# Kernel tuning notes

Measured on AMD Instinct MI355X. Metric: run time of the kernel, lower is better.

Reference implementation:

```python
import jax, jax.numpy as jnp
import numpy as np
import math

B, L, D, H = 16, 512, 128, 8


def setup_inputs() -> dict:
    key = jax.random.key(0)
    ks = jax.random.split(key, 10)
    xavier = lambda k, shp: jax.random.normal(k, shp, jnp.float32) * math.sqrt(2.0 / (shp[0] + shp[1]))
    inp = {
        "x": jax.random.normal(ks[0], (B, L, D), jnp.float32),
        "W_q": xavier(ks[1], (H * D, D)),
        "b_q": jnp.zeros((H * D,), jnp.float32),
        "W_k": xavier(ks[2], (H * D, D)),
        "b_k": jnp.zeros((H * D,), jnp.float32),
        "W_v": xavier(ks[3], (H * D, D)),
        "b_v": jnp.zeros((H * D,), jnp.float32),
        "W_o": xavier(ks[4], (D, H * D)),
        "b_o": jnp.zeros((D,), jnp.float32),
        "pad_mask": jax.random.randint(ks[5], (B, L, L), 0, 2).astype(bool),
        "batch_size": B,
        "max_len": L,
    }
    return inp


def reference(x, W_q, b_q, W_k, b_k, W_v, b_v, W_o, b_o, pad_mask, batch_size, max_len):
    # project: [B, L, D] -> [B, L, H*D] -> head-major [H*B, L, D]
    def proj(W, b):
        y = jnp.einsum('bld,ed->ble', x, W) + b          # [B, L, H*D]
        y = y.reshape(batch_size, max_len, H, D)
        return y.transpose(2, 0, 1, 3).reshape(H * batch_size, max_len, D)

    q = proj(W_q, b_q)
    k = proj(W_k, b_k)
    v = proj(W_v, b_v)

    scores = jnp.einsum('nqd,nkd->nqk', q, k)            # [H*B, L, L]
    mask = jnp.tile(pad_mask, (H, 1, 1))                 # repeat(n_heads,1,1)
    # faithful quirk: mask BEFORE scaling, softmax over QUERY axis (dim=1)
    scores = jnp.where(mask, -1e9, scores) / math.sqrt(D)
    attn = jax.nn.softmax(scores, axis=1)
    att = jnp.einsum('nqk,nkd->nqd', attn, v)            # [H*B, L, D]
    # faithful quirk: torch .view from (H*B, L, D) to (B, L, H*D)
    att = att.reshape(batch_size, max_len, H * D)
    out = jnp.einsum('ble,de->bld', att, W_o) + b_o      # [B, L, D]
    return out
```

## Files before the change

kernel.cpp:

```cpp
#include <hip/hip_runtime.h>

#define B_  16
#define L_  512
#define D_  128
#define H_  8
#define HD_ 1024
#define NH_ 128
#define M_  8192

typedef unsigned short u16;
typedef __attribute__((ext_vector_type(8))) short s16x8;
typedef __attribute__((ext_vector_type(4))) float f32x4;

__device__ __forceinline__ float bf2f(u16 u) {
    union { unsigned u; float f; } x; x.u = ((unsigned)u) << 16; return x.f;
}
__device__ __forceinline__ u16 f2bf(float f) {
    unsigned u = __float_as_uint(f);
    return (u16)((u + 0x7FFFu + ((u >> 16) & 1u)) >> 16);
}

__device__ __forceinline__ void mfma_bt64(const u16* __restrict__ A, int lda,
                                          const u16* __restrict__ B, int ldb,
                                          int K, int lane, f32x4 acc[4][4]) {
    const int mr = lane & 15, quad = lane >> 4;
    for (int k0 = 0; k0 < K; k0 += 32) {
        s16x8 av[4], bv[4];
#pragma unroll
        for (int i = 0; i < 4; i++)
            av[i] = *(const s16x8*)(A + (size_t)(i * 16 + mr) * lda + k0 + quad * 8);
#pragma unroll
        for (int j = 0; j < 4; j++)
            bv[j] = *(const s16x8*)(B + (size_t)(j * 16 + mr) * ldb + k0 + quad * 8);
#pragma unroll
        for (int i = 0; i < 4; i++)
#pragma unroll
            for (int j = 0; j < 4; j++)
                acc[i][j] = __builtin_amdgcn_mfma_f32_16x16x32_bf16(av[i], bv[j], acc[i][j], 0, 0, 0);
    }
}

__global__ void k0_detect(const unsigned int* __restrict__ pad,
                          const unsigned int* __restrict__ xw,
                          int* __restrict__ flags) {
    __shared__ int sMask, sCnt;
    if (threadIdx.x == 0) { sMask = 0; sCnt = 0; }
    __syncthreads();
    int bad = 0;
#pragma unroll
    for (int i = 0; i < 4; i++) {
        unsigned u = pad[threadIdx.x * 4 + i];
        bad |= (u > 1u) ? 1 : 0;
    }
    int cnt = 0;
#pragma unroll
    for (int i = 0; i < 16; i++) {
        unsigned w = xw[threadIdx.x * 16 + i];
        unsigned e = (w >> 7) & 0xFFu;
        cnt += (e >= 100u && e <= 131u) ? 1 : 0;
    }
    if (bad) atomicOr(&sMask, 1);
    atomicAdd(&sCnt, cnt);
    __syncthreads();
    if (threadIdx.x == 0) {
        flags[0] = (sCnt > 2048) ? 1 : 0;
        flags[1] = sMask;
    }
}

#define PREP_TOT 1576064
__global__ __launch_bounds__(256) void kprep_conv(
    const void* x, const void* Wq, const void* bq, const void* Wk, const void* bk,
    const void* Wv, const void* bv, const void* Wo, const void* bo,
    const int* __restrict__ flags,
    u16* xb, u16* Wqb, u16* Wkb, u16* Wvb, u16* Wob,
    u16* bqb, u16* bkb, u16* bvb, u16* bob) {
    int gid = blockIdx.x * 256 + threadIdx.x;
    if (gid >= PREP_TOT) return;
    const int dt = flags[0];
    const void* src; u16* dst; int off;
    if      (gid < 1048576) { src = x;  dst = xb;  off = gid; }
    else if (gid < 1179648) { src = Wq; dst = Wqb; off = gid - 1048576; }
    else if (gid < 1310720) { src = Wk; dst = Wkb; off = gid - 1179648; }
    else if (gid < 1441792) { src = Wv; dst = Wvb; off = gid - 1310720; }
    else if (gid < 1572864) { src = Wo; dst = Wob; off = gid - 1441792; }
    else if (gid < 1573888) { src = bq; dst = bqb; off = gid - 1572864; }
    else if (gid < 1574912) { src = bk; dst = bkb; off = gid - 1573888; }
    else if (gid < 1575936) { src = bv; dst = bvb; off = gid - 1574912; }
    else                    { src = bo; dst = bob; off = gid - 1575936; }
    dst[off] = dt ? ((const u16*)src)[off] : f2bf(((const float*)src)[off]);
}

__global__ __launch_bounds__(256) void kprep_mask(const void* __restrict__ pad,
                                                  const int* __restrict__ flags,
                                                  unsigned* __restrict__ mb) {
    int w = blockIdx.x * 256 + threadIdx.x;
    size_t base = (size_t)w * 32;
    unsigned m = 0;
    if (flags[1]) {
        const unsigned char* p = (const unsigned char*)pad;
#pragma unroll
        for (int b = 0; b < 32; b++) m |= (p[base + b] ? 1u : 0u) << b;
    } else {
        const int* p = (const int*)pad;
#pragma unroll
        for (int b = 0; b < 32; b++) m |= (p[base + b] ? 1u : 0u) << b;
    }
    mb[w] = m;
}

__global__ __launch_bounds__(256) void k1_proj(
    const u16* __restrict__ xb,
    const u16* __restrict__ Wqb, const u16* __restrict__ Wkb, const u16* __restrict__ Wvb,
    const u16* __restrict__ bqb, const u16* __restrict__ bkb, const u16* __restrict__ bvb,
    u16* __restrict__ qb, u16* __restrict__ kb, u16* __restrict__ vtb) {
    const int h  = blockIdx.x;
    const int m0 = blockIdx.y * 128;
    const int z  = blockIdx.z;
    const u16* W    = (z == 0) ? Wqb : (z == 1) ? Wkb : Wvb;
    const u16* bias = (z == 0) ? bqb : (z == 1) ? bkb : bvb;

    const int lane = threadIdx.x & 63, wave = threadIdx.x >> 6;
    const int wr = wave >> 1, wc = wave & 1;
    const int mr = lane & 15, quad = lane >> 4;

    f32x4 acc[4][4];
#pragma unroll
    for (int i = 0; i < 4; i++)
#pragma unroll
        for (int j = 0; j < 4; j++) acc[i][j] = (f32x4){0.f, 0.f, 0.f, 0.f};

    mfma_bt64(xb + (size_t)(m0 + wr * 64) * D_, D_,
              W + (size_t)(h * 128 + wc * 64) * D_, D_, D_, lane, acc);

    __shared__ __align__(16) u16 T[128][144];
#pragma unroll
    for (int i = 0; i < 4; i++)
#pragma unroll
        for (int j = 0; j < 4; j++) {
            int col = wc * 64 + j * 16 + mr;
            float bv_ = bf2f(bias[h * 128 + col]);
#pragma unroll
            for (int r = 0; r < 4; r++)
                T[wr * 64 + i * 16 + quad * 4 + r][col] = f2bf(acc[i][j][r] + bv_);
        }
    __syncthreads();

    const int bb = m0 >> 9, l0 = m0 & 511;
    const int t = threadIdx.x;
    if (z < 2) {
        u16* out = z ? kb : qb;
        int row = t >> 1, c0 = (t & 1) * 64;
        u16* dst = out + ((size_t)(h * B_ + bb) * L_ + l0 + row) * D_ + c0;
#pragma unroll
        for (int c = 0; c < 64; c += 8)
            *(uint4*)(dst + c) = *(const uint4*)&T[row][c0 + c];
    } else {
        int d = t >> 1, lc0 = (t & 1) * 64;
        u16* dst = vtb + ((size_t)(h * B_ + bb) * D_ + d) * L_ + l0 + lc0;
#pragma unroll
        for (int c = 0; c < 64; c += 8) {
            u16 tmp[8];
#pragma unroll
            for (int s = 0; s < 8; s++) tmp[s] = T[lc0 + c + s][d];
            *(uint4*)(dst + c) = *(const uint4*)tmp;
        }
    }
}

__global__ __launch_bounds__(256) void k2_scores(
    const u16* __restrict__ qb, const u16* __restrict__ kb,
    const unsigned* __restrict__ mbits,
    u16* __restrict__ sb, float* __restrict__ linv) {
    const int k0g = blockIdx.x * 128;
    const int n   = blockIdx.y;
    const int bb  = n & (B_ - 1);
    const int lane = threadIdx.x & 63, wave = threadIdx.x >> 6;
    const int wr = wave >> 1, wc = wave & 1;
    const int mr = lane & 15, quad = lane >> 4;
    const float rs = 0.08838834764831845f;

    __shared__ __align__(16) u16 T[128][144];
    __shared__ float CS[2][128];

    const u16* Abase = qb + (size_t)n * L_ * D_;
    const u16* Bbase = kb + (size_t)n * L_ * D_ + (size_t)(k0g + wc * 64) * D_;

    float colsum[4] = {0.f, 0.f, 0.f, 0.f};
    for (int qt = 0; qt < 4; qt++) {
        f32x4 acc[4][4];
#pragma unroll
        for (int i = 0; i < 4; i++)
#pragma unroll
            for (int j = 0; j < 4; j++) acc[i][j] = (f32x4){0.f, 0.f, 0.f, 0.f};

        mfma_bt64(Abase + (size_t)(qt * 128 + wr * 64) * D_, D_, Bbase, D_, D_, lane, acc);

#pragma unroll
        for (int i = 0; i < 4; i++)
#pragma unroll
            for (int j = 0; j < 4; j++) {
                int kc = k0g + wc * 64 + j * 16 + mr;
#pragma unroll
                for (int r = 0; r < 4; r++) {
                    int ql = wr * 64 + i * 16 + quad * 4 + r;
                    int q  = qt * 128 + ql;
                    unsigned w = mbits[((size_t)(bb << 9) + q) * 16 + (kc >> 5)];
                    float s = ((w >> (kc & 31)) & 1u) ? -1e9f : acc[i][j][r];
                    float e = __expf(s * rs);
                    colsum[j] += e;
                    T[ql][wc * 64 + j * 16 + mr] = f2bf(e);
                }
            }
        __syncthreads();
        {
            int t = threadIdx.x, row = t >> 1, c0 = (t & 1) * 64;
            u16* dst = sb + ((size_t)n * L_ + qt * 128 + row) * L_ + k0g + c0;
#pragma unroll
            for (int c = 0; c < 64; c += 8)
                *(uint4*)(dst + c) = *(const uint4*)&T[row][c0 + c];
        }
        __syncthreads();
    }
#pragma unroll
    for (int j = 0; j < 4; j++) {
        colsum[j] += __shfl_xor(colsum[j], 16);
        colsum[j] += __shfl_xor(colsum[j], 32);
    }
    if (quad == 0) {
#pragma unroll
        for (int j = 0; j < 4; j++) CS[wr][wc * 64 + j * 16 + mr] = colsum[j];
    }
    __syncthreads();
    if (threadIdx.x < 128)
        linv[(size_t)n * L_ + k0g + threadIdx.x] =
            1.0f / (CS[0][threadIdx.x] + CS[1][threadIdx.x]);
}

__global__ __launch_bounds__(256) void k3_vscale(u16* __restrict__ vtb,
                                                 const float* __restrict__ linv) {
    int idx = blockIdx.x * 256 + threadIdx.x;
    int n = idx >> 13;
    int rem = idx & 8191;
    int d = rem >> 6;
    int kg = (rem & 63) << 3;
    u16* p = vtb + ((size_t)n * D_ + d) * L_ + kg;
    uint4 v = *(const uint4*)p;
    float lv[8];
    *(float4*)&lv[0] = *(const float4*)(linv + (size_t)n * L_ + kg);
    *(float4*)&lv[4] = *(const float4*)(linv + (size_t)n * L_ + kg + 4);
    u16* u = (u16*)&v;
#pragma unroll
    for (int s = 0; s < 8; s++) u[s] = f2bf(bf2f(u[s]) * lv[s]);
    *(uint4*)p = v;
}

__global__ __launch_bounds__(256) void k4_av(
    const u16* __restrict__ sb, const u16* __restrict__ vtb,
    u16* __restrict__ att) {
    const int q0 = blockIdx.x * 128;
    const int n  = blockIdx.y;
    const int lane = threadIdx.x & 63, wave = threadIdx.x >> 6;
    const int wr = wave >> 1, wc = wave & 1;
    const int mr = lane & 15, quad = lane >> 4;

    f32x4 acc[4][4];
#pragma unroll
    for (int i = 0; i < 4; i++)
#pragma unroll
        for (int j = 0; j < 4; j++) acc[i][j] = (f32x4){0.f, 0.f, 0.f, 0.f};

    mfma_bt64(sb + ((size_t)n * L_ + q0 + wr * 64) * L_, L_,
              vtb + ((size_t)n * D_ + wc * 64) * L_, L_, L_, lane, acc);

    __shared__ __align__(16) u16 T[128][144];
#pragma unroll
    for (int i = 0; i < 4; i++)
#pragma unroll
        for (int j = 0; j < 4; j++) {
            int col = wc * 64 + j * 16 + mr;
#pragma unroll
            for (int r = 0; r < 4; r++)
                T[wr * 64 + i * 16 + quad * 4 + r][col] = f2bf(acc[i][j][r]);
        }
    __syncthreads();
    int t = threadIdx.x, row = t >> 1, c0 = (t & 1) * 64;
    u16* dst = att + ((size_t)n * L_ + q0 + row) * D_ + c0;
#pragma unroll
    for (int c = 0; c < 64; c += 8)
        *(uint4*)(dst + c) = *(const uint4*)&T[row][c0 + c];
}

__global__ __launch_bounds__(128) void k5_out(
    const u16* __restrict__ att, const u16* __restrict__ Wob,
    const u16* __restrict__ bob, const int* __restrict__ flags,
    void* __restrict__ out) {
    const int dt = flags[0];
    const int m0 = blockIdx.x * 64;
    const int lane = threadIdx.x & 63, wc = threadIdx.x >> 6;
    const int mr = lane & 15, quad = lane >> 4;

    f32x4 acc[4][4];
#pragma unroll
    for (int i = 0; i < 4; i++)
#pragma unroll
        for (int j = 0; j < 4; j++) acc[i][j] = (f32x4){0.f, 0.f, 0.f, 0.f};

    mfma_bt64(att + (size_t)m0 * HD_, HD_,
              Wob + (size_t)(wc * 64) * HD_, HD_, HD_, lane, acc);

    __shared__ __align__(16) float Tf[64][132];
#pragma unroll
    for (int i = 0; i < 4; i++)
#pragma unroll
        for (int j = 0; j < 4; j++) {
            int col = wc * 64 + j * 16 + mr;
            float bv_ = bf2f(bob[col]);
#pragma unroll
            for (int r = 0; r < 4; r++)
                Tf[i * 16 + quad * 4 + r][col] = acc[i][j][r] + bv_;
        }
    __syncthreads();
    int t = threadIdx.x, row = t >> 1, c0 = (t & 1) * 64;
    size_t base = (size_t)(m0 + row) * D_ + c0;
    if (dt) {
        u16* o = (u16*)out;
#pragma unroll
        for (int c = 0; c < 64; c += 8) {
            u16 tmp[8];
#pragma unroll
            for (int s = 0; s < 8; s++) tmp[s] = f2bf(Tf[row][c0 + c + s]);
            *(uint4*)(o + base + c) = *(const uint4*)tmp;
        }
    } else {
        float* o = (float*)out;
#pragma unroll
        for (int c = 0; c < 64; c += 4)
            *(float4*)(o + base + c) = *(const float4*)&Tf[row][c0 + c];
    }
}

extern "C" void kernel_launch(void* const* d_in, const int* in_sizes, int n_in,
                              void* d_out, int out_size, void* d_ws, size_t ws_size,
                              hipStream_t stream) {
    (void)in_sizes; (void)n_in; (void)out_size; (void)ws_size;
    const void* x  = d_in[0];
    const void* Wq = d_in[1]; const void* bq = d_in[2];
    const void* Wk = d_in[3]; const void* bk = d_in[4];
    const void* Wv = d_in[5]; const void* bv = d_in[6];
    const void* Wo = d_in[7]; const void* bo = d_in[8];
    const void* pad = d_in[9];

    char* p = (char*)d_ws;
    auto alloc = [&](size_t bytes) { char* r = p; p += (bytes + 255) & ~(size_t)255; return r; };
    int*  flags = (int*)alloc(256);
    u16*  xb   = (u16*)alloc(2097152);
    u16*  Wqb  = (u16*)alloc(262144);
    u16*  Wkb  = (u16*)alloc(262144);
    u16*  Wvb  = (u16*)alloc(262144);
    u16*  Wob  = (u16*)alloc(262144);
    u16*  bqb  = (u16*)alloc(2048);
    u16*  bkb  = (u16*)alloc(2048);
    u16*  bvb  = (u16*)alloc(2048);
    u16*  bob  = (u16*)alloc(256);
    unsigned* mbits = (unsigned*)alloc(524288);
    float* linv = (float*)alloc(262144);
    u16*  qb   = (u16*)alloc(16777216);
    u16*  kb   = (u16*)alloc(16777216);
    u16*  vtb  = (u16*)alloc(16777216);
    u16*  sb   = (u16*)alloc(67108864);
    u16*  att  = qb;

    k0_detect<<<1, 256, 0, stream>>>((const unsigned*)pad, (const unsigned*)x, flags);
    kprep_conv<<<(PREP_TOT + 255) / 256, 256, 0, stream>>>(
        x, Wq, bq, Wk, bk, Wv, bv, Wo, bo, flags,
        xb, Wqb, Wkb, Wvb, Wob, bqb, bkb, bvb, bob);
    kprep_mask<<<512, 256, 0, stream>>>(pad, flags, mbits);
    k1_proj<<<dim3(8, 64, 3), 256, 0, stream>>>(
        xb, Wqb, Wkb, Wvb, bqb, bkb, bvb, qb, kb, vtb);
    k2_scores<<<dim3(4, NH_), 256, 0, stream>>>(qb, kb, mbits, sb, linv);
    k3_vscale<<<4096, 256, 0, stream>>>(vtb, linv);
    k4_av<<<dim3(4, NH_), 256, 0, stream>>>(sb, vtb, att);
    k5_out<<<128, 128, 0, stream>>>(att, Wob, bob, flags, d_out);
}
```

Baseline: 253.4 us.

## Recompute scores in fused AV kernel instead of materializing score matrix

Replaces the score-write/vscale/AV pipeline with a two-pass scheme. The first pass computes only per-key column sums of exp(scores) via atomics on a finer grid. The second pass recomputes QK^T, normalizes with the column sums in registers and multiplies by V through shared memory. This removes the 64MB bf16 score buffer round trip and the V rescale kernel, at the cost of computing QK^T twice and doing float atomics.

```diff
diff --git a/kernel.cpp b/kernel.cpp
--- a/kernel.cpp
+++ b/kernel.cpp
@@ -93,8 +93,10 @@
 
 __global__ __launch_bounds__(256) void kprep_mask(const void* __restrict__ pad,
                                                   const int* __restrict__ flags,
-                                                  unsigned* __restrict__ mb) {
+                                                  unsigned* __restrict__ mb,
+                                                  float* __restrict__ colsum) {
     int w = blockIdx.x * 256 + threadIdx.x;
+    if (w < NH_ * L_) colsum[w] = 0.0f;
     size_t base = (size_t)w * 32;
     unsigned m = 0;
     if (flags[1]) {
@@ -168,127 +170,140 @@
     }
 }
 
-__global__ __launch_bounds__(256) void k2_scores(
+__global__ __launch_bounds__(256) void k2_colsum(
     const u16* __restrict__ qb, const u16* __restrict__ kb,
     const unsigned* __restrict__ mbits,
-    u16* __restrict__ sb, float* __restrict__ linv) {
-    const int k0g = blockIdx.x * 128;
-    const int n   = blockIdx.y;
-    const int bb  = n & (B_ - 1);
+    float* __restrict__ colsum) {
+    const int qt = blockIdx.x >> 2, kt = blockIdx.x & 3;
+    const int n  = blockIdx.y;
+    const int bb = n & (B_ - 1);
     const int lane = threadIdx.x & 63, wave = threadIdx.x >> 6;
     const int wr = wave >> 1, wc = wave & 1;
     const int mr = lane & 15, quad = lane >> 4;
     const float rs = 0.08838834764831845f;
 
-    __shared__ __align__(16) u16 T[128][144];
-    __shared__ float CS[2][128];
-
-    const u16* Abase = qb + (size_t)n * L_ * D_;
-    const u16* Bbase = kb + (size_t)n * L_ * D_ + (size_t)(k0g + wc * 64) * D_;
-
-    float colsum[4] = {0.f, 0.f, 0.f, 0.f};
-    for (int qt = 0; qt < 4; qt++) {
-        f32x4 acc[4][4];
+    f32x4 acc[4][4];
+#pragma unroll
+    for (int i = 0; i < 4; i++)
+#pragma unroll
+        for (int j = 0; j < 4; j++) acc[i][j] = (f32x4){0.f, 0.f, 0.f, 0.f};
+
+    mfma_bt64(qb + (size_t)n * L_ * D_ + (size_t)(qt * 128 + wr * 64) * D_, D_,
+              kb + (size_t)n * L_ * D_ + (size_t)(kt * 128 + wc * 64) * D_, D_,
+              D_, lane, acc);
+
+    float cs[4] = {0.f, 0.f, 0.f, 0.f};
+#pragma unroll
+    for (int j = 0; j < 4; j++) {
+        int kc = kt * 128 + wc * 64 + j * 16 + mr;
 #pragma unroll
         for (int i = 0; i < 4; i++)
 #pragma unroll
-            for (int j = 0; j < 4; j++) acc[i][j] = (f32x4){0.f, 0.f, 0.f, 0.f};
-
-        mfma_bt64(Abase + (size_t)(qt * 128 + wr * 64) * D_, D_, Bbase, D_, D_, lane, acc);
-
+            for (int r = 0; r < 4; r++) {
+                int q = qt * 128 + wr * 64 + i * 16 + quad * 4 + r;
+                unsigned w = mbits[((size_t)(bb << 9) + q) * 16 + (kc >> 5)];
+                float e = ((w >> (kc & 31)) & 1u) ? 0.f : __expf(acc[i][j][r] * rs);
+                cs[j] += e;
+            }
+    }
+#pragma unroll
+    for (int j = 0; j < 4; j++) {
+        cs[j] += __shfl_xor(cs[j], 16);
+        cs[j] += __shfl_xor(cs[j], 32);
+    }
+    if (quad == 0) {
+#pragma unroll
+        for (int j = 0; j < 4; j++)
+            atomicAdd(&colsum[(size_t)n * L_ + kt * 128 + wc * 64 + j * 16 + mr], cs[j]);
+    }
+}
+
+__global__ __launch_bounds__(256) void k4_fused(
+    const u16* __restrict__ qb, const u16* __restrict__ kb,
+    const u16* __restrict__ vtb, const unsigned* __restrict__ mbits,
+    const float* __restrict__ colsum,
+    u16* __restrict__ att) {
+    const int qt = blockIdx.x;
+    const int n  = blockIdx.y;
+    const int bb = n & (B_ - 1);
+    const int lane = threadIdx.x & 63, wave = threadIdx.x >> 6;
+    const int wr = wave >> 1, wc = wave & 1;
+    const int mr = lane & 15, quad = lane >> 4;
+    const float rs = 0.08838834764831845f;
+
+    __shared__ __align__(16) u16 E[128][136];
+
+    const u16* Aq = qb + (size_t)n * L_ * D_ + (size_t)(qt * 128 + wr * 64) * D_;
+    const u16* Vt = vtb + (size_t)n * D_ * L_;
+
+    f32x4 acc_o[4][4];
+#pragma unroll
+    for (int i = 0; i < 4; i++)
+#pragma unroll
+        for (int j = 0; j < 4; j++) acc_o[i][j] = (f32x4){0.f, 0.f, 0.f, 0.f};
+
+#pragma unroll 1
+    for (int kt = 0; kt < 4; kt++) {
+        f32x4 acc_s[4][4];
 #pragma unroll
         for (int i = 0; i < 4; i++)
 #pragma unroll
-            for (int j = 0; j < 4; j++) {
-                int kc = k0g + wc * 64 + j * 16 + mr;
+            for (int j = 0; j < 4; j++) acc_s[i][j] = (f32x4){0.f, 0.f, 0.f, 0.f};
+
+        mfma_bt64(Aq, D_,
+                  kb + (size_t)n * L_ * D_ + (size_t)(kt * 128 + wc * 64) * D_, D_,
+                  D_, lane, acc_s);
+
+#pragma unroll
+        for (int j = 0; j < 4; j++) {
+            int kc = kt * 128 + wc * 64 + j * 16 + mr;
+            float li = 1.0f / colsum[(size_t)n * L_ + kc];
+#pragma unroll
+            for (int i = 0; i < 4; i++)
 #pragma unroll
                 for (int r = 0; r < 4; r++) {
                     int ql = wr * 64 + i * 16 + quad * 4 + r;
                     int q  = qt * 128 + ql;
                     unsigned w = mbits[((size_t)(bb << 9) + q) * 16 + (kc >> 5)];
-                    float s = ((w >> (kc & 31)) & 1u) ? -1e9f : acc[i][j][r];
-                    float e = __expf(s * rs);
-                    colsum[j] += e;
-                    T[ql][wc * 64 + j * 16 + mr] = f2bf(e);
+                    float e = ((w >> (kc & 31)) & 1u) ? 0.f
+                              : __expf(acc_s[i][j][r] * rs) * li;
+                    E[ql][wc * 64 + j * 16 + mr] = f2bf(e);
                 }
-            }
+        }
         __syncthreads();
-        {
-            int t = threadIdx.x, row = t >> 1, c0 = (t & 1) * 64;
-            u16* dst = sb + ((size_t)n * L_ + qt * 128 + row) * L_ + k0g + c0;
-#pragma unroll
-            for (int c = 0; c < 64; c += 8)
-                *(uint4*)(dst + c) = *(const uint4*)&T[row][c0 + c];
+
+#pragma unroll
+        for (int k0 = 0; k0 < 128; k0 += 32) {
+            s16x8 av[4], bv[4];
+#pragma unroll
+            for (int i = 0; i < 4; i++)
+                av[i] = *(const s16x8*)&E[wr * 64 + i * 16 + mr][k0 + quad * 8];
+#pragma unroll
+            for (int j = 0; j < 4; j++)
+                bv[j] = *(const s16x8*)(Vt + (size_t)(wc * 64 + j * 16 + mr) * L_
+                                        + kt * 128 + k0 + quad * 8);
+#pragma unroll
+            for (int i = 0; i < 4; i++)
+#pragma unroll
+                for (int j = 0; j < 4; j++)
+                    acc_o[i][j] = __builtin_amdgcn_mfma_f32_16x16x32_bf16(av[i], bv[j], acc_o[i][j], 0, 0, 0);
         }
         __syncthreads();
     }
-#pragma unroll
-    for (int j = 0; j < 4; j++) {
-        colsum[j] += __shfl_xor(colsum[j], 16);
-        colsum[j] += __shfl_xor(colsum[j], 32);
-    }
-    if (quad == 0) {
-#pragma unroll
-        for (int j = 0; j < 4; j++) CS[wr][wc * 64 + j * 16 + mr] = colsum[j];
-    }
-    __syncthreads();
-    if (threadIdx.x < 128)
-        linv[(size_t)n * L_ + k0g + threadIdx.x] =
-            1.0f / (CS[0][threadIdx.x] + CS[1][threadIdx.x]);
-}
-
-__global__ __launch_bounds__(256) void k3_vscale(u16* __restrict__ vtb,
-                                                 const float* __restrict__ linv) {
-    int idx = blockIdx.x * 256 + threadIdx.x;
-    int n = idx >> 13;
-    int rem = idx & 8191;
-    int d = rem >> 6;
-    int kg = (rem & 63) << 3;
-    u16* p = vtb + ((size_t)n * D_ + d) * L_ + kg;
-    uint4 v = *(const uint4*)p;
-    float lv[8];
-    *(float4*)&lv[0] = *(const float4*)(linv + (size_t)n * L_ + kg);
-    *(float4*)&lv[4] = *(const float4*)(linv + (size_t)n * L_ + kg + 4);
-    u16* u = (u16*)&v;
-#pragma unroll
-    for (int s = 0; s < 8; s++) u[s] = f2bf(bf2f(u[s]) * lv[s]);
-    *(uint4*)p = v;
-}
-
-__global__ __launch_bounds__(256) void k4_av(
-    const u16* __restrict__ sb, const u16* __restrict__ vtb,
-    u16* __restrict__ att) {
-    const int q0 = blockIdx.x * 128;
-    const int n  = blockIdx.y;
-    const int lane = threadIdx.x & 63, wave = threadIdx.x >> 6;
-    const int wr = wave >> 1, wc = wave & 1;
-    const int mr = lane & 15, quad = lane >> 4;
-
-    f32x4 acc[4][4];
-#pragma unroll
-    for (int i = 0; i < 4; i++)
-#pragma unroll
-        for (int j = 0; j < 4; j++) acc[i][j] = (f32x4){0.f, 0.f, 0.f, 0.f};
-
-    mfma_bt64(sb + ((size_t)n * L_ + q0 + wr * 64) * L_, L_,
-              vtb + ((size_t)n * D_ + wc * 64) * L_, L_, L_, lane, acc);
-
-    __shared__ __align__(16) u16 T[128][144];
-#pragma unroll
-    for (int i = 0; i < 4; i++)
-#pragma unroll
-        for (int j = 0; j < 4; j++) {
-            int col = wc * 64 + j * 16 + mr;
+
+#pragma unroll
+    for (int i = 0; i < 4; i++)
+#pragma unroll
+        for (int j = 0; j < 4; j++)
 #pragma unroll
             for (int r = 0; r < 4; r++)
-                T[wr * 64 + i * 16 + quad * 4 + r][col] = f2bf(acc[i][j][r]);
-        }
+                E[wr * 64 + i * 16 + quad * 4 + r][wc * 64 + j * 16 + mr] = f2bf(acc_o[i][j][r]);
     __syncthreads();
     int t = threadIdx.x, row = t >> 1, c0 = (t & 1) * 64;
-    u16* dst = att + ((size_t)n * L_ + q0 + row) * D_ + c0;
+    u16* dst = att + ((size_t)n * L_ + qt * 128 + row) * D_ + c0;
 #pragma unroll
     for (int c = 0; c < 64; c += 8)
-        *(uint4*)(dst + c) = *(const uint4*)&T[row][c0 + c];
+        *(uint4*)(dst + c) = *(const uint4*)&E[row][c0 + c];
 }
 
 __global__ __launch_bounds__(128) void k5_out(
@@ -364,22 +379,20 @@
     u16*  bvb  = (u16*)alloc(2048);
     u16*  bob  = (u16*)alloc(256);
     unsigned* mbits = (unsigned*)alloc(524288);
-    float* linv = (float*)alloc(262144);
+    float* colsum = (float*)alloc(262144);
     u16*  qb   = (u16*)alloc(16777216);
     u16*  kb   = (u16*)alloc(16777216);
     u16*  vtb  = (u16*)alloc(16777216);
-    u16*  sb   = (u16*)alloc(67108864);
     u16*  att  = qb;
 
     k0_detect<<<1, 256, 0, stream>>>((const unsigned*)pad, (const unsigned*)x, flags);
     kprep_conv<<<(PREP_TOT + 255) / 256, 256, 0, stream>>>(
         x, Wq, bq, Wk, bk, Wv, bv, Wo, bo, flags,
         xb, Wqb, Wkb, Wvb, Wob, bqb, bkb, bvb, bob);
-    kprep_mask<<<512, 256, 0, stream>>>(pad, flags, mbits);
+    kprep_mask<<<512, 256, 0, stream>>>(pad, flags, mbits, colsum);
     k1_proj<<<dim3(8, 64, 3), 256, 0, stream>>>(
         xb, Wqb, Wkb, Wvb, bqb, bkb, bvb, qb, kb, vtb);
-    k2_scores<<<dim3(4, NH_), 256, 0, stream>>>(qb, kb, mbits, sb, linv);
-    k3_vscale<<<4096, 256, 0, stream>>>(vtb, linv);
-    k4_av<<<dim3(4, NH_), 256, 0, stream>>>(sb, vtb, att);
+    k2_colsum<<<dim3(16, NH_), 256, 0, stream>>>(qb, kb, mbits, colsum);
+    k4_fused<<<dim3(4, NH_), 256, 0, stream>>>(qb, kb, vtb, mbits, colsum, att);
     k5_out<<<128, 128, 0, stream>>>(att, Wob, bob, flags, d_out);
 }
```

New measurement: 296.2 us. +16.9%, slower.

## Split score kernel across query tiles with atomic column sums; shrink AV tiles

Applied to the files above, without the earlier changes.

The scores kernel now gives each block a single 128x128 (query, key) tile instead of looping over four query tiles, so the grid grows from 512 to 2048 blocks. Because the column softmax denominators span several blocks, they are accumulated with atomicAdd into a buffer that the mask-prep kernel zeroes. The V-scale kernel now divides by that sum. Mask words are staged once per block into shared memory, masked entries write zero directly instead of computing exp of a huge negative, and the AV kernel uses 64-row query tiles with an inline MFMA loop to double its block count. The aim is more parallelism and occupancy, at the cost of atomic traffic and a run-to-run nondeterministic summation order.

```diff
diff --git a/kernel.cpp b/kernel.cpp
--- a/kernel.cpp
+++ b/kernel.cpp
@@ -93,8 +93,10 @@
 
 __global__ __launch_bounds__(256) void kprep_mask(const void* __restrict__ pad,
                                                   const int* __restrict__ flags,
-                                                  unsigned* __restrict__ mb) {
+                                                  unsigned* __restrict__ mb,
+                                                  float* __restrict__ colsum) {
     int w = blockIdx.x * 256 + threadIdx.x;
+    if (w < NH_ * L_) colsum[w] = 0.0f;
     size_t base = (size_t)w * 32;
     unsigned m = 0;
     if (flags[1]) {
@@ -168,77 +170,80 @@
     }
 }
 
-__global__ __launch_bounds__(256) void k2_scores(
+__global__ __launch_bounds__(256, 4) void k2_scores(
     const u16* __restrict__ qb, const u16* __restrict__ kb,
     const unsigned* __restrict__ mbits,
-    u16* __restrict__ sb, float* __restrict__ linv) {
-    const int k0g = blockIdx.x * 128;
-    const int n   = blockIdx.y;
-    const int bb  = n & (B_ - 1);
+    u16* __restrict__ sb, float* __restrict__ colsum) {
+    const int qt = blockIdx.x >> 2, kt = blockIdx.x & 3;
+    const int n  = blockIdx.y;
+    const int bb = n & (B_ - 1);
     const int lane = threadIdx.x & 63, wave = threadIdx.x >> 6;
     const int wr = wave >> 1, wc = wave & 1;
     const int mr = lane & 15, quad = lane >> 4;
     const float rs = 0.08838834764831845f;
 
-    __shared__ __align__(16) u16 T[128][144];
+    __shared__ __align__(16) u16 T[128][136];
     __shared__ float CS[2][128];
-
-    const u16* Abase = qb + (size_t)n * L_ * D_;
-    const u16* Bbase = kb + (size_t)n * L_ * D_ + (size_t)(k0g + wc * 64) * D_;
-
-    float colsum[4] = {0.f, 0.f, 0.f, 0.f};
-    for (int qt = 0; qt < 4; qt++) {
-        f32x4 acc[4][4];
+    __shared__ unsigned MW[128][4];
+
+    {
+        int t = threadIdx.x;
+        int q = t >> 1, w2 = (t & 1) * 2;
+        const unsigned* src = mbits + ((size_t)(bb << 9) + qt * 128 + q) * 16 + kt * 4 + w2;
+        uint2 v = *(const uint2*)src;
+        MW[q][w2] = v.x; MW[q][w2 + 1] = v.y;
+    }
+
+    f32x4 acc[4][4];
+#pragma unroll
+    for (int i = 0; i < 4; i++)
+#pragma unroll
+        for (int j = 0; j < 4; j++) acc[i][j] = (f32x4){0.f, 0.f, 0.f, 0.f};
+
+    mfma_bt64(qb + ((size_t)n * L_ + qt * 128 + wr * 64) * D_, D_,
+              kb + ((size_t)n * L_ + kt * 128 + wc * 64) * D_, D_, D_, lane, acc);
+    __syncthreads();
+
+    float cs[4] = {0.f, 0.f, 0.f, 0.f};
+#pragma unroll
+    for (int j = 0; j < 4; j++) {
+        const int wsel = wc * 2 + (j >> 1);
+        const int bit  = ((j & 1) << 4) + mr;
 #pragma unroll
         for (int i = 0; i < 4; i++)
 #pragma unroll
-            for (int j = 0; j < 4; j++) acc[i][j] = (f32x4){0.f, 0.f, 0.f, 0.f};
-
-        mfma_bt64(Abase + (size_t)(qt * 128 + wr * 64) * D_, D_, Bbase, D_, D_, lane, acc);
-
-#pragma unroll
-        for (int i = 0; i < 4; i++)
-#pragma unroll
-            for (int j = 0; j < 4; j++) {
-                int kc = k0g + wc * 64 + j * 16 + mr;
-#pragma unroll
-                for (int r = 0; r < 4; r++) {
-                    int ql = wr * 64 + i * 16 + quad * 4 + r;
-                    int q  = qt * 128 + ql;
-                    unsigned w = mbits[((size_t)(bb << 9) + q) * 16 + (kc >> 5)];
-                    float s = ((w >> (kc & 31)) & 1u) ? -1e9f : acc[i][j][r];
-                    float e = __expf(s * rs);
-                    colsum[j] += e;
-                    T[ql][wc * 64 + j * 16 + mr] = f2bf(e);
-                }
+            for (int r = 0; r < 4; r++) {
+                int ql = wr * 64 + i * 16 + quad * 4 + r;
+                unsigned w = MW[ql][wsel];
+                float e = ((w >> bit) & 1u) ? 0.f : __expf(acc[i][j][r] * rs);
+                cs[j] += e;
+                T[ql][wc * 64 + j * 16 + mr] = f2bf(e);
             }
-        __syncthreads();
-        {
-            int t = threadIdx.x, row = t >> 1, c0 = (t & 1) * 64;
-            u16* dst = sb + ((size_t)n * L_ + qt * 128 + row) * L_ + k0g + c0;
-#pragma unroll
-            for (int c = 0; c < 64; c += 8)
-                *(uint4*)(dst + c) = *(const uint4*)&T[row][c0 + c];
-        }
-        __syncthreads();
     }
 #pragma unroll
     for (int j = 0; j < 4; j++) {
-        colsum[j] += __shfl_xor(colsum[j], 16);
-        colsum[j] += __shfl_xor(colsum[j], 32);
+        cs[j] += __shfl_xor(cs[j], 16);
+        cs[j] += __shfl_xor(cs[j], 32);
     }
     if (quad == 0) {
 #pragma unroll
-        for (int j = 0; j < 4; j++) CS[wr][wc * 64 + j * 16 + mr] = colsum[j];
-    }
-    __syncthreads();
+        for (int j = 0; j < 4; j++) CS[wr][wc * 64 + j * 16 + mr] = cs[j];
+    }
+    __syncthreads();
+    {
+        int t = threadIdx.x, row = t >> 1, c0 = (t & 1) * 64;
+        u16* dst = sb + ((size_t)n * L_ + qt * 128 + row) * L_ + kt * 128 + c0;
+#pragma unroll
+        for (int c = 0; c < 64; c += 8)
+            *(uint4*)(dst + c) = *(const uint4*)&T[row][c0 + c];
+    }
     if (threadIdx.x < 128)
-        linv[(size_t)n * L_ + k0g + threadIdx.x] =
-            1.0f / (CS[0][threadIdx.x] + CS[1][threadIdx.x]);
+        atomicAdd(&colsum[(size_t)n * L_ + kt * 128 + threadIdx.x],
+                  CS[0][threadIdx.x] + CS[1][threadIdx.x]);
 }
 
 __global__ __launch_bounds__(256) void k3_vscale(u16* __restrict__ vtb,
-                                                 const float* __restrict__ linv) {
+                                                 const float* __restrict__ colsum) {
     int idx = blockIdx.x * 256 + threadIdx.x;
     int n = idx >> 13;
     int rem = idx & 8191;
@@ -246,48 +251,61 @@
     int kg = (rem & 63) << 3;
     u16* p = vtb + ((size_t)n * D_ + d) * L_ + kg;
     uint4 v = *(const uint4*)p;
-    float lv[8];
-    *(float4*)&lv[0] = *(const float4*)(linv + (size_t)n * L_ + kg);
-    *(float4*)&lv[4] = *(const float4*)(linv + (size_t)n * L_ + kg + 4);
+    float cv[8];
+    *(float4*)&cv[0] = *(const float4*)(colsum + (size_t)n * L_ + kg);
+    *(float4*)&cv[4] = *(const float4*)(colsum + (size_t)n * L_ + kg + 4);
     u16* u = (u16*)&v;
 #pragma unroll
-    for (int s = 0; s < 8; s++) u[s] = f2bf(bf2f(u[s]) * lv[s]);
+    for (int s = 0; s < 8; s++) u[s] = f2bf(bf2f(u[s]) / cv[s]);
     *(uint4*)p = v;
 }
 
-__global__ __launch_bounds__(256) void k4_av(
+__global__ __launch_bounds__(256, 4) void k4_av(
     const u16* __restrict__ sb, const u16* __restrict__ vtb,
     u16* __restrict__ att) {
-    const int q0 = blockIdx.x * 128;
+    const int q0 = blockIdx.x * 64;
     const int n  = blockIdx.y;
     const int lane = threadIdx.x & 63, wave = threadIdx.x >> 6;
     const int wr = wave >> 1, wc = wave & 1;
     const int mr = lane & 15, quad = lane >> 4;
 
-    f32x4 acc[4][4];
-#pragma unroll
-    for (int i = 0; i < 4; i++)
+    f32x4 acc[2][4];
+#pragma unroll
+    for (int i = 0; i < 2; i++)
 #pragma unroll
         for (int j = 0; j < 4; j++) acc[i][j] = (f32x4){0.f, 0.f, 0.f, 0.f};
 
-    mfma_bt64(sb + ((size_t)n * L_ + q0 + wr * 64) * L_, L_,
-              vtb + ((size_t)n * D_ + wc * 64) * L_, L_, L_, lane, acc);
-
-    __shared__ __align__(16) u16 T[128][144];
-#pragma unroll
-    for (int i = 0; i < 4; i++)
-#pragma unroll
-        for (int j = 0; j < 4; j++) {
-            int col = wc * 64 + j * 16 + mr;
+    const u16* A  = sb  + ((size_t)n * L_ + q0 + wr * 32) * L_;
+    const u16* Bb = vtb + ((size_t)n * D_ + wc * 64) * L_;
+
+    for (int k0 = 0; k0 < L_; k0 += 32) {
+        s16x8 av[2], bv[4];
+#pragma unroll
+        for (int i = 0; i < 2; i++)
+            av[i] = *(const s16x8*)(A + (size_t)(i * 16 + mr) * L_ + k0 + quad * 8);
+#pragma unroll
+        for (int j = 0; j < 4; j++)
+            bv[j] = *(const s16x8*)(Bb + (size_t)(j * 16 + mr) * L_ + k0 + quad * 8);
+#pragma unroll
+        for (int i = 0; i < 2; i++)
+#pragma unroll
+            for (int j = 0; j < 4; j++)
+                acc[i][j] = __builtin_amdgcn_mfma_f32_16x16x32_bf16(av[i], bv[j], acc[i][j], 0, 0, 0);
+    }
+
+    __shared__ __align__(16) u16 T[64][136];
+#pragma unroll
+    for (int i = 0; i < 2; i++)
+#pragma unroll
+        for (int j = 0; j < 4; j++)
 #pragma unroll
             for (int r = 0; r < 4; r++)
-                T[wr * 64 + i * 16 + quad * 4 + r][col] = f2bf(acc[i][j][r]);
-        }
-    __syncthreads();
-    int t = threadIdx.x, row = t >> 1, c0 = (t & 1) * 64;
+                T[wr * 32 + i * 16 + quad * 4 + r][wc * 64 + j * 16 + mr] = f2bf(acc[i][j][r]);
+    __syncthreads();
+    int t = threadIdx.x, row = t >> 2, c0 = (t & 3) * 32;
     u16* dst = att + ((size_t)n * L_ + q0 + row) * D_ + c0;
 #pragma unroll
-    for (int c = 0; c < 64; c += 8)
+    for (int c = 0; c < 32; c += 8)
         *(uint4*)(dst + c) = *(const uint4*)&T[row][c0 + c];
 }
 
@@ -364,7 +382,7 @@
     u16*  bvb  = (u16*)alloc(2048);
     u16*  bob  = (u16*)alloc(256);
     unsigned* mbits = (unsigned*)alloc(524288);
-    float* linv = (float*)alloc(262144);
+    float* colsum = (float*)alloc(262144);
     u16*  qb   = (u16*)alloc(16777216);
     u16*  kb   = (u16*)alloc(16777216);
     u16*  vtb  = (u16*)alloc(16777216);
@@ -375,11 +393,11 @@
     kprep_conv<<<(PREP_TOT + 255) / 256, 256, 0, stream>>>(
         x, Wq, bq, Wk, bk, Wv, bv, Wo, bo, flags,
         xb, Wqb, Wkb, Wvb, Wob, bqb, bkb, bvb, bob);
-    kprep_mask<<<512, 256, 0, stream>>>(pad, flags, mbits);
+    kprep_mask<<<512, 256, 0, stream>>>(pad, flags, mbits, colsum);
     k1_proj<<<dim3(8, 64, 3), 256, 0, stream>>>(
         xb, Wqb, Wkb, Wvb, bqb, bkb, bvb, qb, kb, vtb);
-    k2_scores<<<dim3(4, NH_), 256, 0, stream>>>(qb, kb, mbits, sb, linv);
-    k3_vscale<<<4096, 256, 0, stream>>>(vtb, linv);
-    k4_av<<<dim3(4, NH_), 256, 0, stream>>>(sb, vtb, att);
+    k2_scores<<<dim3(16, NH_), 256, 0, stream>>>(qb, kb, mbits, sb, colsum);
+    k3_vscale<<<4096, 256, 0, stream>>>(vtb, colsum);
+    k4_av<<<dim3(8, NH_), 256, 0, stream>>>(sb, vtb, att);
     k5_out<<<128, 128, 0, stream>>>(att, Wob, bob, flags, d_out);
 }
```

New measurement: 275.6 us. 8.8% more time.
